# Kernel tuning notes

Measured on AMD Instinct MI355X. Metric: run time of the kernel, lower is better.

## Reference

```python
import jax, jax.numpy as jnp
import numpy as np
from jax import lax

H = 1024
W = 1024
WIN = 32
STR = 16
NH = (H - WIN) // STR + 1  # 63
N = NH * NH                # 3969 patches
DN3 = ('NCDHW', 'OIDHW', 'NCDHW')
DN2 = ('NCHW', 'OIHW', 'NCHW')


def setup_inputs() -> dict:
    key = jax.random.key(0)
    ks = jax.random.split(key, 13)
    r = lambda k, s, sc=0.05: jax.random.normal(k, s, dtype=jnp.float32) * sc
    return {
        'x1': jax.random.normal(ks[0], (1, 1, 1, H, W), jnp.float32),
        'x2': jax.random.normal(ks[1], (1, 1, 1, H, W), jnp.float32),
        'conv1_w': r(ks[2], (24, 1, 2, 8, 8)),      # Conv3d(1,24,(2,8,8)) [O,I,D,H,W]
        'conv1_b': r(ks[3], (24,)),
        'conv2_w': r(ks[4], (60, 24, 5, 5)),         # Conv2d(24,60,5)
        'conv2_b': r(ks[5], (60,)),
        'deconv2_w': r(ks[6], (60, 24, 5, 5)),       # ConvTranspose2d(60,24,5) [I,O,kH,kW]
        'deconv2_b': r(ks[7], (24,)),
        'deconv1_w': r(ks[8], (24, 1, 2, 8, 8)),     # ConvTranspose3d(24,1,(2,8,8)) [I,O,D,H,W]
        'deconv1_b': r(ks[9], (1,)),
        'lin_w': r(ks[10], (N, 2), 0.5),             # per-patch Linear(2,1) weights
        'lin_b': r(ks[11], (N,), 0.5),               # per-patch Linear(2,1) bias
        'linear1_w': r(ks[12], (1, 1), 0.5),         # Linear(1,1,bias=False)
    }


def _conv(x, w, b, dn):
    nd = w.ndim - 2
    y = lax.conv_general_dilated(x, w, (1,) * nd, 'VALID', dimension_numbers=dn)
    return y + b.reshape((1, -1) + (1,) * nd)


def _convT(x, w, b, dn):
    # stride-1, pad-0 transposed conv == full-pad conv with flipped, IO-swapped kernel
    nd = w.ndim - 2
    wf = jnp.flip(w, axis=tuple(range(2, w.ndim))).swapaxes(0, 1)  # [O,I,*k]
    pad = [(k - 1, k - 1) for k in w.shape[2:]]
    y = lax.conv_general_dilated(x, wf, (1,) * nd, pad, dimension_numbers=dn)
    return y + b.reshape((1, -1) + (1,) * nd)


def reference(x1, x2, conv1_w, conv1_b, conv2_w, conv2_b, deconv2_w, deconv2_b,
              deconv1_w, deconv1_b, lin_w, lin_b, linear1_w):
    x = jnp.concatenate([x1, x2], axis=2)[0, 0]  # [2,H,W]
    idx = (jnp.arange(NH) * STR)[:, None] + jnp.arange(WIN)[None, :]  # [NH,32]
    # unfold dims 3,4 with window 32 / stride 16 -> [2,NH,NW,32,32]
    patches = x[:, idx[:, None, :, None], idx[None, :, None, :]]
    outX = patches.reshape(2, N, WIN, WIN).transpose(1, 0, 2, 3)[:, None]  # [N,1,2,32,32]
    h = jax.nn.elu(_conv(outX, conv1_w, conv1_b, DN3))        # [N,24,1,25,25]
    h = jax.nn.relu(_conv(h[:, :, 0], conv2_w, conv2_b, DN2))  # [N,60,21,21]
    h = jax.nn.elu(_convT(h, deconv2_w, deconv2_b, DN2))       # [N,24,25,25]
    h = _convT(h[:, :, None], deconv1_w, deconv1_b, DN3)       # [N,1,2,32,32]
    # per-patch Linear(2,1) over depth channels, batched over all patches
    p = jnp.einsum('nchw,nc->nhw', h[:, 0], lin_w) + lin_b[:, None, None]  # [N,32,32]
    p = p.reshape(NH, NH, WIN, WIN)
    # col2im: overlap-add fold, block 32, stride 16 -> [H,W]
    recon = jnp.zeros((H, W), jnp.float32).at[idx[:, None, :, None], idx[None, :, None, :]].add(p)
    outX2 = recon * linear1_w[0, 0]  # Linear(1,1,bias=False) per pixel
    return x2 - outX2.reshape(x2.shape)
```

## Files before the change

### kernel.cpp

```cpp
#include <hip/hip_runtime.h>
#include <hip/hip_bf16.h>

static constexpr int H_ = 1024;
static constexpr int W_ = 1024;
static constexpr int STR_ = 16;
static constexpr int NH_ = 63;
static constexpr int NPATCH_ = NH_ * NH_;

typedef short bf16x8 __attribute__((ext_vector_type(8)));
typedef short short4v __attribute__((ext_vector_type(4)));
typedef float f32x4 __attribute__((ext_vector_type(4)));

static constexpr int SH1_STRIDE = 48;
static constexpr int SH2_BASE   = 30016;
static constexpr int SH2_STRIDE = 120;
static constexpr int ZROW_REL   = 441 * SH2_STRIDE;
static constexpr int SPB0       = 30016;
static constexpr int SPB1       = 35136;
static constexpr int SWC_BASE   = 30016;
static constexpr int SP_ACC     = 34112;
static constexpr int LDS_BYTES  = 83072;

__device__ __forceinline__ unsigned short f2bf(float x) {
    __hip_bfloat16 b = __float2bfloat16(x);
    return __builtin_bit_cast(unsigned short, b);
}

__device__ __forceinline__ f32x4 mfma_bf16(bf16x8 a, bf16x8 b, f32x4 c) {
    return __builtin_amdgcn_mfma_f32_16x16x32_bf16(a, b, c, 0, 0, 0);
}

__global__ __launch_bounds__(1024, 4) void fused_patch_kernel(
    const float* __restrict__ x1, const float* __restrict__ x2,
    const float* __restrict__ c1b, const float* __restrict__ c2b,
    const float* __restrict__ d2b, const float* __restrict__ d1b,
    const float* __restrict__ lin_w, const float* __restrict__ lin_b,
    const unsigned short* __restrict__ w1frag,
    const unsigned short* __restrict__ w2frag,
    const unsigned short* __restrict__ dw2frag,
    const float* __restrict__ dw1,
    float* __restrict__ recon)
{
    __shared__ alignas(16) char sbuf[LDS_BYTES];
    const int n  = blockIdx.x;
    const int t  = (int)threadIdx.x;
    const int pi = n / NH_, pj = n % NH_;
    const int Y0 = pi * STR_, X0 = pj * STR_;
    const int wv = t >> 6, lane = t & 63;
    const int ln15 = lane & 15, quad = lane >> 4;

    if (t < 30) ((float*)(sbuf + SH2_BASE + ZROW_REL))[t] = 0.f;
    for (int k = t; k < 2048; k += 1024) {
        int d = k >> 10, r = k & 1023, y = r >> 5, x = r & 31;
        unsigned short b = f2bf((d ? x2 : x1)[(Y0 + y) * W_ + (X0 + x)]);
        int row = (d * 32 + y) * 40;
        ((unsigned short*)(sbuf + SPB0))[row + x] = b;
        if (x > 0) ((unsigned short*)(sbuf + SPB1))[row + x - 1] = b;
    }
    __syncthreads();

    for (int tl = wv; tl < 50; tl += 16) {
        const int vcol = tl >> 1, ubase = (tl & 1) * 16;
        const int u = ubase + ln15;
        const char* abase = sbuf + ((vcol & 1) ? SPB1 : SPB0) + (vcol & ~1) * 2;
        f32x4 acc[2];
        acc[0] = (f32x4){0.f, 0.f, 0.f, 0.f};
        acc[1] = (f32x4){0.f, 0.f, 0.f, 0.f};
        #pragma unroll
        for (int kc = 0; kc < 4; ++kc) {
            const int idx8 = kc * 4 + quad;
            const int dd = idx8 >> 3, pp = idx8 & 7;
            const unsigned int* ap = (const unsigned int*)(abase + (dd * 32 + u + pp) * 80);
            union { unsigned int u4[4]; bf16x8 v; } af;
            af.u4[0] = ap[0]; af.u4[1] = ap[1]; af.u4[2] = ap[2]; af.u4[3] = ap[3];
            bf16x8 b0 = *(const bf16x8*)(w1frag + (((kc * 2 + 0) * 64) + lane) * 8);
            bf16x8 b1 = *(const bf16x8*)(w1frag + (((kc * 2 + 1) * 64) + lane) * 8);
            acc[0] = mfma_bf16(af.v, b0, acc[0]);
            acc[1] = mfma_bf16(af.v, b1, acc[1]);
        }
        #pragma unroll
        for (int ntp = 0; ntp < 2; ++ntp) {
            const int c = ntp * 16 + ln15;
            if (c < 24) {
                const float bias = c1b[c];
                #pragma unroll
                for (int r = 0; r < 4; ++r) {
                    int uu = ubase + quad * 4 + r;
                    if (uu < 25) {
                        float hv = acc[ntp][r] + bias;
                        hv = hv > 0.f ? hv : expm1f(hv);
                        *(unsigned short*)(sbuf + (uu * 25 + vcol) * SH1_STRIDE + c * 2) = f2bf(hv);
                    }
                }
            }
        }
    }
    __syncthreads();

    if (wv < 14) {
        int abase2[2];
        #pragma unroll
        for (int i = 0; i < 2; ++i) {
            int m = (wv + i * 14) * 16 + ln15;
            if (m > 440) m = 440;
            abase2[i] = ((m / 21) * 25 + (m % 21)) * SH1_STRIDE;
        }
        float bias[4];
        #pragma unroll
        for (int nt = 0; nt < 4; ++nt) {
            int o = nt * 16 + ln15;
            bias[nt] = (o < 60) ? c2b[o] : 0.f;
        }
        f32x4 acc2[2][4];
        #pragma unroll
        for (int i = 0; i < 2; ++i)
            #pragma unroll
            for (int nt = 0; nt < 4; ++nt)
                acc2[i][nt] = (f32x4){0.f, 0.f, 0.f, 0.f};

        const unsigned short* wb = w2frag + lane * 8;
        #pragma unroll
        for (int p = 0; p < 5; ++p) {
            #pragma unroll
            for (int q = 0; q < 5; ++q) {
                const int tap  = p * 5 + q;
                const int toff = (p * 25 + q) * SH1_STRIDE;
                bf16x8 b[4];
                #pragma unroll
                for (int nt = 0; nt < 4; ++nt)
                    b[nt] = *(const bf16x8*)(wb + (tap * 4 + nt) * 512);
                #pragma unroll
                for (int i = 0; i < 2; ++i) {
                    bf16x8 a = *(const bf16x8*)(sbuf + abase2[i] + toff + quad * 16);
                    #pragma unroll
                    for (int nt = 0; nt < 4; ++nt)
                        acc2[i][nt] = mfma_bf16(a, b[nt], acc2[i][nt]);
                }
            }
        }
        #pragma unroll
        for (int i = 0; i < 2; ++i) {
            #pragma unroll
            for (int r = 0; r < 4; ++r) {
                int pix = (wv + i * 14) * 16 + quad * 4 + r;
                if (pix < 441) {
                    unsigned short* rowp = (unsigned short*)(sbuf + SH2_BASE + pix * SH2_STRIDE);
                    #pragma unroll
                    for (int nt = 0; nt < 4; ++nt) {
                        int o = nt * 16 + ln15;
                        if (o < 60)
                            rowp[o] = f2bf(fmaxf(acc2[i][nt][r] + bias[nt], 0.f));
                    }
                }
            }
        }
    }
    __syncthreads();

    f32x4 acc3[3][2];
    {
        #pragma unroll
        for (int i = 0; i < 3; ++i) {
            acc3[i][0] = (f32x4){0.f, 0.f, 0.f, 0.f};
            acc3[i][1] = (f32x4){0.f, 0.f, 0.f, 0.f};
        }
        int uarr[3], varr[3], a120[3];
        bool mval[3];
        #pragma unroll
        for (int i = 0; i < 3; ++i) {
            int m = (wv + i * 16) * 16 + ln15;
            mval[i] = (m < 625);
            int mc = mval[i] ? m : 0;
            uarr[i] = mc / 25; varr[i] = mc % 25;
            a120[i] = (uarr[i] * 21 + varr[i]) * SH2_STRIDE;
        }
        const unsigned short* db = dw2frag + lane * 8;
        #pragma unroll
        for (int dy = 0; dy < 5; ++dy) {
            #pragma unroll
            for (int dx = 0; dx < 5; ++dx) {
                const int tap   = dy * 5 + dx;
                const int t2off = (dy * 21 + dx) * SH2_STRIDE;
                bf16x8 b00 = *(const bf16x8*)(db + tap * 2048);
                bf16x8 b01 = *(const bf16x8*)(db + tap * 2048 + 512);
                bf16x8 b10 = *(const bf16x8*)(db + tap * 2048 + 1024);
                bf16x8 b11 = *(const bf16x8*)(db + tap * 2048 + 1536);
                #pragma unroll
                for (int i = 0; i < 3; ++i) {
                    if (i == 2 && wv >= 8) continue;
                    int yv = uarr[i] - dy, xv = varr[i] - dx;
                    bool ok = mval[i] && ((unsigned)yv < 21u) && ((unsigned)xv < 21u);
                    int ra = ok ? (a120[i] - t2off) : ZROW_REL;
                    const char* ap = sbuf + SH2_BASE + ra + quad * 16;
                    short4v lo0 = *(const short4v*)(ap);
                    short4v hi0 = *(const short4v*)(ap + 8);
                    bf16x8 a0 = __builtin_shufflevector(lo0, hi0, 0, 1, 2, 3, 4, 5, 6, 7);
                    acc3[i][0] = mfma_bf16(a0, b00, acc3[i][0]);
                    acc3[i][1] = mfma_bf16(a0, b01, acc3[i][1]);
                    short4v lo1 = *(const short4v*)(ap + 64);
                    short4v hi1 = *(const short4v*)(ap + 72);
                    bf16x8 a1 = __builtin_shufflevector(lo1, hi1, 0, 1, 2, 3, 4, 5, 6, 7);
                    acc3[i][0] = mfma_bf16(a1, b10, acc3[i][0]);
                    acc3[i][1] = mfma_bf16(a1, b11, acc3[i][1]);
                }
            }
        }
    }
    __syncthreads();

    const float lw0 = lin_w[2 * n], lw1 = lin_w[2 * n + 1];
    float* sp = (float*)(sbuf + SP_ACC);
    {
        const int c0 = ln15, c1 = 16 + ln15;
        const float db0 = d2b[c0];
        const float db1 = (c1 < 24) ? d2b[c1] : 0.f;
        #pragma unroll
        for (int i = 0; i < 3; ++i) {
            if (i == 2 && wv >= 8) continue;
            #pragma unroll
            for (int r = 0; r < 4; ++r) {
                int pix = (wv + i * 16) * 16 + quad * 4 + r;
                if (pix < 625) {
                    unsigned short* rowp = (unsigned short*)(sbuf + pix * SH1_STRIDE);
                    float hv = acc3[i][0][r] + db0;
                    rowp[c0] = f2bf(hv > 0.f ? hv : expm1f(hv));
                    if (c1 < 24) {
                        float hw = acc3[i][1][r] + db1;
                        rowp[c1] = f2bf(hw > 0.f ? hw : expm1f(hw));
                    }
                }
            }
        }
    }
    for (int k = t; k < 2048; k += 1024) {
        int r = k >> 5, c = k & 31;
        float v = 0.f;
        if (c < 24)
            v = lw0 * dw1[(c * 2 + 0) * 64 + r] + lw1 * dw1[(c * 2 + 1) * 64 + r];
        ((unsigned short*)(sbuf + SWC_BASE))[r * 32 + c] = f2bf(v);
    }
    sp[t] = 0.f;
    __syncthreads();

    {
        bf16x8 wbv[4];
        #pragma unroll
        for (int nt = 0; nt < 4; ++nt)
            wbv[nt] = *(const bf16x8*)(sbuf + SWC_BASE + (nt * 16 + ln15) * 64 + quad * 16);
        #pragma unroll
        for (int i = 0; i < 3; ++i) {
            int mt = wv + i * 16;
            if (mt >= 40) continue;
            int m = mt * 16 + ln15;
            if (m > 624) m = 624;
            bf16x8 a = *(const bf16x8*)(sbuf + m * SH1_STRIDE + quad * 16);
            #pragma unroll
            for (int nt = 0; nt < 4; ++nt) {
                f32x4 acc4 = (f32x4){0.f, 0.f, 0.f, 0.f};
                acc4 = mfma_bf16(a, wbv[nt], acc4);
                #pragma unroll
                for (int r = 0; r < 4; ++r) {
                    int pix = mt * 16 + quad * 4 + r;
                    if (pix < 625) {
                        int u = pix / 25, v = pix % 25;
                        int rv = nt * 16 + ln15;
                        atomicAdd(&sp[(u + (rv >> 3)) * 32 + v + (rv & 7)], acc4[r]);
                    }
                }
            }
        }
    }
    __syncthreads();

    const float obias = d1b[0] * (lw0 + lw1) + lin_b[n];
    {
        int yy = t >> 5, xx = t & 31;
        atomicAdd(&recon[(Y0 + yy) * W_ + (X0 + xx)], sp[t] + obias);
    }
}

__global__ void prep_kernel(const float* __restrict__ c1w,
                            const float* __restrict__ c2w,
                            const float* __restrict__ d2w,
                            unsigned short* __restrict__ w1frag,
                            unsigned short* __restrict__ w2frag,
                            unsigned short* __restrict__ dw2frag)
{
    int i = blockIdx.x * blockDim.x + threadIdx.x;
    if (i < 51200) {
        int j = i & 7, lane = (i >> 3) & 63;
        int ln15 = lane & 15, quad = lane >> 4;
        if (i < 4096) {
            int g = i >> 9;
            int kc = g >> 1, nt = g & 1;
            int nn = nt * 16 + ln15, k = kc * 32 + quad * 8 + j;
            w1frag[i] = f2bf((nn < 24) ? c1w[nn * 128 + k] : 0.f);
        }
        {
            int nt = (i >> 9) & 3, tap = i >> 11;
            int o = nt * 16 + ln15, c = quad * 8 + j;
            float v = (o < 60 && c < 24) ? c2w[(o * 24 + c) * 25 + tap] : 0.f;
            w2frag[i] = f2bf(v);
        }
        {
            int nt = (i >> 9) & 1, kc = (i >> 10) & 1, tap = i >> 11;
            int k = kc * 32 + quad * 8 + j, c = nt * 16 + ln15;
            float v = (k < 60 && c < 24) ? d2w[(k * 24 + c) * 25 + tap] : 0.f;
            dw2frag[i] = f2bf(v);
        }
    }
}

__global__ void finalize_kernel(const float* __restrict__ x2,
                                const float* __restrict__ l1w,
                                float* __restrict__ out)
{
    int i = blockIdx.x * blockDim.x + threadIdx.x;
    if (i < H_ * W_) {
        float r = out[i];
        out[i] = x2[i] - r * l1w[0];
    }
}

extern "C" void kernel_launch(void* const* d_in, const int* in_sizes, int n_in,
                              void* d_out, int out_size, void* d_ws, size_t ws_size,
                              hipStream_t stream)
{
    const float* x1  = (const float*)d_in[0];
    const float* x2  = (const float*)d_in[1];
    const float* c1w = (const float*)d_in[2];
    const float* c1b = (const float*)d_in[3];
    const float* c2w = (const float*)d_in[4];
    const float* c2b = (const float*)d_in[5];
    const float* d2w = (const float*)d_in[6];
    const float* d2b = (const float*)d_in[7];
    const float* d1w = (const float*)d_in[8];
    const float* d1b = (const float*)d_in[9];
    const float* lw  = (const float*)d_in[10];
    const float* lb  = (const float*)d_in[11];
    const float* l1w = (const float*)d_in[12];

    float*          out     = (float*)d_out;
    unsigned short* w1frag  = (unsigned short*)d_ws;
    unsigned short* w2frag  = (unsigned short*)((char*)d_ws + 8192);
    unsigned short* dw2frag = (unsigned short*)((char*)d_ws + 110592);

    hipMemsetAsync(d_out, 0, (size_t)H_ * W_ * sizeof(float), stream);
    prep_kernel<<<100, 512, 0, stream>>>(c1w, c2w, d2w, w1frag, w2frag, dw2frag);
    fused_patch_kernel<<<NPATCH_, 1024, 0, stream>>>(x1, x2, c1b, c2b, d2b, d1b,
                                                     lw, lb, w1frag, w2frag, dw2frag,
                                                     d1w, out);
    finalize_kernel<<<(H_ * W_ + 255) / 256, 256, 0, stream>>>(x2, l1w, out);
}
```

Baseline: 1.435 ms.

## Compute conv1 once over full image and stream it to per-patch kernel

Adds a kernel that computes the first conv+ELU over the whole image into a global bf16 workspace, removing the fourfold redundant conv1 work across overlapping patches. The per-patch kernel then reads conv2 inputs directly from global memory, uses 512 threads and a smaller LDS footprint. The new path runs only when the workspace is large enough; otherwise the old fused kernel is used. It trades recomputation for about 50MB of extra global traffic and uncached-LDS reads in conv2.

New measurement: 3.090 ms. 2.15x slower.

```diff
diff --git a/kernel.cpp b/kernel.cpp
--- a/kernel.cpp
+++ b/kernel.cpp
@@ -6,31 +6,298 @@
 static constexpr int STR_ = 16;
 static constexpr int NH_ = 63;
 static constexpr int NPATCH_ = NH_ * NH_;
+static constexpr int HO_ = 1017;
 
 typedef short bf16x8 __attribute__((ext_vector_type(8)));
 typedef short short4v __attribute__((ext_vector_type(4)));
 typedef float f32x4 __attribute__((ext_vector_type(4)));
 
-static constexpr int SH1_STRIDE = 48;
-static constexpr int SH2_BASE   = 30016;
-static constexpr int SH2_STRIDE = 120;
-static constexpr int ZROW_REL   = 441 * SH2_STRIDE;
-static constexpr int SPB0       = 30016;
-static constexpr int SPB1       = 35136;
-static constexpr int SWC_BASE   = 30016;
-static constexpr int SP_ACC     = 34112;
-static constexpr int LDS_BYTES  = 83072;
+static constexpr size_t WS_FRAGS   = 212992;
+static constexpr int    H1_XSTRIDE = 48;
+static constexpr int    H1_YSTRIDE = 1024 * 48;
+static constexpr size_t H1_BYTES   = (size_t)HO_ * H1_YSTRIDE;
+static constexpr size_t WS_NEED_A  = WS_FRAGS + H1_BYTES;
 
 __device__ __forceinline__ unsigned short f2bf(float x) {
     __hip_bfloat16 b = __float2bfloat16(x);
     return __builtin_bit_cast(unsigned short, b);
 }
-
 __device__ __forceinline__ f32x4 mfma_bf16(bf16x8 a, bf16x8 b, f32x4 c) {
     return __builtin_amdgcn_mfma_f32_16x16x32_bf16(a, b, c, 0, 0, 0);
 }
 
-__global__ __launch_bounds__(1024, 4) void fused_patch_kernel(
+
+__global__ __launch_bounds__(512, 4) void conv1_full_kernel(
+    const float* __restrict__ x1, const float* __restrict__ x2,
+    const float* __restrict__ c1b,
+    const unsigned short* __restrict__ w1frag,
+    unsigned short* __restrict__ h1full)
+{
+    __shared__ alignas(16) unsigned short spb[2 * 2 * 39 * 40];
+    unsigned short* copy0 = spb;
+    unsigned short* copy1 = spb + 2 * 39 * 40;
+
+    const int b  = blockIdx.x;
+    const int by = b >> 5, bx = b & 31;
+    const int y0 = by * 32, x0 = bx * 32;
+    const int t  = (int)threadIdx.x;
+    const int wv = t >> 6, lane = t & 63;
+    const int ln15 = lane & 15, quad = lane >> 4;
+
+    for (int k = t; k < 2 * 39 * 39; k += 512) {
+        int d = k / 1521, r = k % 1521, yy = r / 39, xx = r % 39;
+        int gy = y0 + yy; if (gy > 1023) gy = 1023;
+        int gx = x0 + xx; if (gx > 1023) gx = 1023;
+        unsigned short v = f2bf((d ? x2 : x1)[gy * W_ + gx]);
+        int row = (d * 39 + yy) * 40;
+        copy0[row + xx] = v;
+        if (xx > 0) copy1[row + xx - 1] = v;
+    }
+    __syncthreads();
+
+    bf16x8 bw[4][2];
+    #pragma unroll
+    for (int kc = 0; kc < 4; ++kc)
+        #pragma unroll
+        for (int nt = 0; nt < 2; ++nt)
+            bw[kc][nt] = *(const bf16x8*)(w1frag + (((kc * 2 + nt) * 64) + lane) * 8);
+
+    for (int tl = wv; tl < 64; tl += 8) {
+        const int vcol = tl >> 1, ubase = (tl & 1) * 16;
+        const int u = ubase + ln15;
+        const char* abase = (const char*)((vcol & 1) ? copy1 : copy0) + (vcol & ~1) * 2;
+        f32x4 acc[2];
+        acc[0] = (f32x4){0.f, 0.f, 0.f, 0.f};
+        acc[1] = (f32x4){0.f, 0.f, 0.f, 0.f};
+        #pragma unroll
+        for (int kc = 0; kc < 4; ++kc) {
+            const int idx8 = kc * 4 + quad;
+            const int dd = idx8 >> 3, pp = idx8 & 7;
+            const unsigned int* ap = (const unsigned int*)(abase + (dd * 39 + u + pp) * 80);
+            union { unsigned int u4[4]; bf16x8 v; } af;
+            af.u4[0] = ap[0]; af.u4[1] = ap[1]; af.u4[2] = ap[2]; af.u4[3] = ap[3];
+            acc[0] = mfma_bf16(af.v, bw[kc][0], acc[0]);
+            acc[1] = mfma_bf16(af.v, bw[kc][1], acc[1]);
+        }
+        const int xg = x0 + vcol;
+        #pragma unroll
+        for (int ntp = 0; ntp < 2; ++ntp) {
+            const int c = ntp * 16 + ln15;
+            if (c < 24) {
+                const float bias = c1b[c];
+                #pragma unroll
+                for (int r = 0; r < 4; ++r) {
+                    int yg = y0 + ubase + quad * 4 + r;
+                    if (yg < HO_ && xg < HO_) {
+                        float hv = acc[ntp][r] + bias;
+                        hv = hv > 0.f ? hv : expm1f(hv);
+                        h1full[(yg * 1024 + xg) * 24 + c] = f2bf(hv);
+                    }
+                }
+            }
+        }
+    }
+}
+
+static constexpr int A_SH2_STRIDE = 120;
+static constexpr int A_ZROW  = 52920;
+static constexpr int A_SWC   = 53056;
+static constexpr int A_SP    = 57152;
+static constexpr int A_LDS   = 61248;
+static constexpr int A_H3STR = 48;
+
+__global__ __launch_bounds__(512, 4) void fused_patch_global(
+    const float* __restrict__ c2b, const float* __restrict__ d2b,
+    const float* __restrict__ d1b,
+    const float* __restrict__ lin_w, const float* __restrict__ lin_b,
+    const unsigned short* __restrict__ h1full,
+    const unsigned short* __restrict__ w2frag,
+    const unsigned short* __restrict__ dw2frag,
+    const float* __restrict__ dw1,
+    float* __restrict__ recon)
+{
+    __shared__ alignas(16) char sbuf[A_LDS];
+    const int n  = blockIdx.x;
+    const int t  = (int)threadIdx.x;
+    const int pi = n / NH_, pj = n % NH_;
+    const int Y0 = pi * STR_, X0 = pj * STR_;
+    const int wv = t >> 6, lane = t & 63;
+    const int ln15 = lane & 15, quad = lane >> 4;
+
+    if (t < 34) ((float*)(sbuf + A_ZROW))[t] = 0.f;
+
+    float bias2[4];
+    #pragma unroll
+    for (int nt = 0; nt < 4; ++nt) {
+        int o = nt * 16 + ln15;
+        bias2[nt] = (o < 60) ? c2b[o] : 0.f;
+    }
+    for (int mt = wv; mt < 28; mt += 8) {
+        int m = mt * 16 + ln15;
+        if (m > 440) m = 440;
+        int hy = m / 21, hx = m % 21;
+        const char* abase = (const char*)h1full
+                          + ((Y0 + hy) * 1024 + (X0 + hx)) * H1_XSTRIDE + quad * 16;
+        f32x4 acc[4];
+        #pragma unroll
+        for (int nt = 0; nt < 4; ++nt) acc[nt] = (f32x4){0.f, 0.f, 0.f, 0.f};
+        const unsigned short* wb = w2frag + lane * 8;
+        #pragma unroll
+        for (int p = 0; p < 5; ++p) {
+            #pragma unroll
+            for (int q = 0; q < 5; ++q) {
+                const int tap = p * 5 + q;
+                bf16x8 a = *(const bf16x8*)(abase + p * H1_YSTRIDE + q * H1_XSTRIDE);
+                #pragma unroll
+                for (int nt = 0; nt < 4; ++nt) {
+                    bf16x8 bb = *(const bf16x8*)(wb + (tap * 4 + nt) * 512);
+                    acc[nt] = mfma_bf16(a, bb, acc[nt]);
+                }
+            }
+        }
+        #pragma unroll
+        for (int r = 0; r < 4; ++r) {
+            int pix = mt * 16 + quad * 4 + r;
+            if (pix < 441) {
+                unsigned short* rowp = (unsigned short*)(sbuf + pix * A_SH2_STRIDE);
+                #pragma unroll
+                for (int nt = 0; nt < 4; ++nt) {
+                    int o = nt * 16 + ln15;
+                    if (o < 60)
+                        rowp[o] = f2bf(fmaxf(acc[nt][r] + bias2[nt], 0.f));
+                }
+            }
+        }
+    }
+    __syncthreads();
+
+    f32x4 acc3[5][2];
+    {
+        int uarr[5], varr[5], a120[5];
+        bool mval[5];
+        #pragma unroll
+        for (int i = 0; i < 5; ++i) {
+            acc3[i][0] = (f32x4){0.f, 0.f, 0.f, 0.f};
+            acc3[i][1] = (f32x4){0.f, 0.f, 0.f, 0.f};
+            int m = (wv + i * 8) * 16 + ln15;
+            mval[i] = (m < 625);
+            int mc = mval[i] ? m : 0;
+            uarr[i] = mc / 25; varr[i] = mc % 25;
+            a120[i] = (uarr[i] * 21 + varr[i]) * A_SH2_STRIDE;
+        }
+        const unsigned short* db = dw2frag + lane * 8;
+        #pragma unroll
+        for (int dy = 0; dy < 5; ++dy) {
+            #pragma unroll
+            for (int dx = 0; dx < 5; ++dx) {
+                const int tap   = dy * 5 + dx;
+                const int t2off = (dy * 21 + dx) * A_SH2_STRIDE;
+                bf16x8 b00 = *(const bf16x8*)(db + tap * 2048);
+                bf16x8 b01 = *(const bf16x8*)(db + tap * 2048 + 512);
+                bf16x8 b10 = *(const bf16x8*)(db + tap * 2048 + 1024);
+                bf16x8 b11 = *(const bf16x8*)(db + tap * 2048 + 1536);
+                #pragma unroll
+                for (int i = 0; i < 5; ++i) {
+                    int yv = uarr[i] - dy, xv = varr[i] - dx;
+                    bool ok = mval[i] && ((unsigned)yv < 21u) && ((unsigned)xv < 21u);
+                    int ra = ok ? (a120[i] - t2off) : A_ZROW;
+                    const char* ap = sbuf + ra + quad * 16;
+                    short4v lo0 = *(const short4v*)(ap);
+                    short4v hi0 = *(const short4v*)(ap + 8);
+                    bf16x8 a0 = __builtin_shufflevector(lo0, hi0, 0, 1, 2, 3, 4, 5, 6, 7);
+                    acc3[i][0] = mfma_bf16(a0, b00, acc3[i][0]);
+                    acc3[i][1] = mfma_bf16(a0, b01, acc3[i][1]);
+                    short4v lo1 = *(const short4v*)(ap + 64);
+                    short4v hi1 = *(const short4v*)(ap + 72);
+                    bf16x8 a1 = __builtin_shufflevector(lo1, hi1, 0, 1, 2, 3, 4, 5, 6, 7);
+                    acc3[i][0] = mfma_bf16(a1, b10, acc3[i][0]);
+                    acc3[i][1] = mfma_bf16(a1, b11, acc3[i][1]);
+                }
+            }
+        }
+    }
+    __syncthreads();
+
+    const float lw0 = lin_w[2 * n], lw1 = lin_w[2 * n + 1];
+    float* sp = (float*)(sbuf + A_SP);
+    {
+        const int c0 = ln15, c1 = 16 + ln15;
+        const float db0 = d2b[c0];
+        const float db1 = (c1 < 24) ? d2b[c1] : 0.f;
+        #pragma unroll
+        for (int i = 0; i < 5; ++i) {
+            #pragma unroll
+            for (int r = 0; r < 4; ++r) {
+                int pix = (wv + i * 8) * 16 + quad * 4 + r;
+                if (pix < 625) {
+                    unsigned short* rowp = (unsigned short*)(sbuf + pix * A_H3STR);
+                    float hv = acc3[i][0][r] + db0;
+                    rowp[c0] = f2bf(hv > 0.f ? hv : expm1f(hv));
+                    if (c1 < 24) {
+                        float hw = acc3[i][1][r] + db1;
+                        rowp[c1] = f2bf(hw > 0.f ? hw : expm1f(hw));
+                    }
+                }
+            }
+        }
+    }
+    for (int k = t; k < 2048; k += 512) {
+        int r = k >> 5, c = k & 31;
+        float v = 0.f;
+        if (c < 24)
+            v = lw0 * dw1[(c * 2 + 0) * 64 + r] + lw1 * dw1[(c * 2 + 1) * 64 + r];
+        ((unsigned short*)(sbuf + A_SWC))[r * 32 + c] = f2bf(v);
+    }
+    for (int k = t; k < 1024; k += 512) sp[k] = 0.f;
+    __syncthreads();
+
+    {
+        bf16x8 wbv[4];
+        #pragma unroll
+        for (int nt = 0; nt < 4; ++nt)
+            wbv[nt] = *(const bf16x8*)(sbuf + A_SWC + (nt * 16 + ln15) * 64 + quad * 16);
+        #pragma unroll
+        for (int i = 0; i < 5; ++i) {
+            int mt = wv + i * 8;
+            int m = mt * 16 + ln15;
+            if (m > 624) m = 624;
+            bf16x8 a = *(const bf16x8*)(sbuf + m * A_H3STR + quad * 16);
+            #pragma unroll
+            for (int nt = 0; nt < 4; ++nt) {
+                f32x4 acc4 = (f32x4){0.f, 0.f, 0.f, 0.f};
+                acc4 = mfma_bf16(a, wbv[nt], acc4);
+                #pragma unroll
+                for (int r = 0; r < 4; ++r) {
+                    int pix = mt * 16 + quad * 4 + r;
+                    if (pix < 625) {
+                        int u = pix / 25, v = pix % 25;
+                        int rv = nt * 16 + ln15;
+                        atomicAdd(&sp[(u + (rv >> 3)) * 32 + v + (rv & 7)], acc4[r]);
+                    }
+                }
+            }
+        }
+    }
+    __syncthreads();
+
+    const float obias = d1b[0] * (lw0 + lw1) + lin_b[n];
+    for (int k = t; k < 1024; k += 512) {
+        int yy = k >> 5, xx = k & 31;
+        atomicAdd(&recon[(Y0 + yy) * W_ + (X0 + xx)], sp[k] + obias);
+    }
+}
+
+static constexpr int B_SH1_STRIDE = 48;
+static constexpr int B_SH2_BASE   = 30016;
+static constexpr int B_SH2_STRIDE = 120;
+static constexpr int B_ZROW_REL   = 441 * B_SH2_STRIDE;
+static constexpr int B_SPB0       = 30016;
+static constexpr int B_SPB1       = 35136;
+static constexpr int B_SWC_BASE   = 30016;
+static constexpr int B_SP_ACC     = 34112;
+static constexpr int B_LDS_BYTES  = 83072;
+
+__global__ __launch_bounds__(1024, 4) void fused_patch_local(
     const float* __restrict__ x1, const float* __restrict__ x2,
     const float* __restrict__ c1b, const float* __restrict__ c2b,
     const float* __restrict__ d2b, const float* __restrict__ d1b,
@@ -41,7 +308,7 @@
     const float* __restrict__ dw1,
     float* __restrict__ recon)
 {
-    __shared__ alignas(16) char sbuf[LDS_BYTES];
+    __shared__ alignas(16) char sbuf[B_LDS_BYTES];
     const int n  = blockIdx.x;
     const int t  = (int)threadIdx.x;
     const int pi = n / NH_, pj = n % NH_;
@@ -49,20 +316,20 @@
     const int wv = t >> 6, lane = t & 63;
     const int ln15 = lane & 15, quad = lane >> 4;
 
-    if (t < 30) ((float*)(sbuf + SH2_BASE + ZROW_REL))[t] = 0.f;
+    if (t < 30) ((float*)(sbuf + B_SH2_BASE + B_ZROW_REL))[t] = 0.f;
     for (int k = t; k < 2048; k += 1024) {
         int d = k >> 10, r = k & 1023, y = r >> 5, x = r & 31;
         unsigned short b = f2bf((d ? x2 : x1)[(Y0 + y) * W_ + (X0 + x)]);
         int row = (d * 32 + y) * 40;
-        ((unsigned short*)(sbuf + SPB0))[row + x] = b;
-        if (x > 0) ((unsigned short*)(sbuf + SPB1))[row + x - 1] = b;
+        ((unsigned short*)(sbuf + B_SPB0))[row + x] = b;
+        if (x > 0) ((unsigned short*)(sbuf + B_SPB1))[row + x - 1] = b;
     }
     __syncthreads();
 
     for (int tl = wv; tl < 50; tl += 16) {
         const int vcol = tl >> 1, ubase = (tl & 1) * 16;
         const int u = ubase + ln15;
-        const char* abase = sbuf + ((vcol & 1) ? SPB1 : SPB0) + (vcol & ~1) * 2;
+        const char* abase = sbuf + ((vcol & 1) ? B_SPB1 : B_SPB0) + (vcol & ~1) * 2;
         f32x4 acc[2];
         acc[0] = (f32x4){0.f, 0.f, 0.f, 0.f};
         acc[1] = (f32x4){0.f, 0.f, 0.f, 0.f};
@@ -89,7 +356,7 @@
                     if (uu < 25) {
                         float hv = acc[ntp][r] + bias;
                         hv = hv > 0.f ? hv : expm1f(hv);
-                        *(unsigned short*)(sbuf + (uu * 25 + vcol) * SH1_STRIDE + c * 2) = f2bf(hv);
+                        *(unsigned short*)(sbuf + (uu * 25 + vcol) * B_SH1_STRIDE + c * 2) = f2bf(hv);
                     }
                 }
             }
@@ -103,7 +370,7 @@
         for (int i = 0; i < 2; ++i) {
             int m = (wv + i * 14) * 16 + ln15;
             if (m > 440) m = 440;
-            abase2[i] = ((m / 21) * 25 + (m % 21)) * SH1_STRIDE;
+            abase2[i] = ((m / 21) * 25 + (m % 21)) * B_SH1_STRIDE;
         }
         float bias[4];
         #pragma unroll
@@ -124,7 +391,7 @@
             #pragma unroll
             for (int q = 0; q < 5; ++q) {
                 const int tap  = p * 5 + q;
-                const int toff = (p * 25 + q) * SH1_STRIDE;
+                const int toff = (p * 25 + q) * B_SH1_STRIDE;
                 bf16x8 b[4];
                 #pragma unroll
                 for (int nt = 0; nt < 4; ++nt)
@@ -144,7 +411,7 @@
             for (int r = 0; r < 4; ++r) {
                 int pix = (wv + i * 14) * 16 + quad * 4 + r;
                 if (pix < 441) {
-                    unsigned short* rowp = (unsigned short*)(sbuf + SH2_BASE + pix * SH2_STRIDE);
+                    unsigned short* rowp = (unsigned short*)(sbuf + B_SH2_BASE + pix * B_SH2_STRIDE);
                     #pragma unroll
                     for (int nt = 0; nt < 4; ++nt) {
                         int o = nt * 16 + ln15;
@@ -172,7 +439,7 @@
             mval[i] = (m < 625);
             int mc = mval[i] ? m : 0;
             uarr[i] = mc / 25; varr[i] = mc % 25;
-            a120[i] = (uarr[i] * 21 + varr[i]) * SH2_STRIDE;
+            a120[i] = (uarr[i] * 21 + varr[i]) * B_SH2_STRIDE;
         }
         const unsigned short* db = dw2frag + lane * 8;
         #pragma unroll
@@ -180,7 +447,7 @@
             #pragma unroll
             for (int dx = 0; dx < 5; ++dx) {
                 const int tap   = dy * 5 + dx;
-                const int t2off = (dy * 21 + dx) * SH2_STRIDE;
+                const int t2off = (dy * 21 + dx) * B_SH2_STRIDE;
                 bf16x8 b00 = *(const bf16x8*)(db + tap * 2048);
                 bf16x8 b01 = *(const bf16x8*)(db + tap * 2048 + 512);
                 bf16x8 b10 = *(const bf16x8*)(db + tap * 2048 + 1024);
@@ -190,8 +457,8 @@
                     if (i == 2 && wv >= 8) continue;
                     int yv = uarr[i] - dy, xv = varr[i] - dx;
                     bool ok = mval[i] && ((unsigned)yv < 21u) && ((unsigned)xv < 21u);
-                    int ra = ok ? (a120[i] - t2off) : ZROW_REL;
-                    const char* ap = sbuf + SH2_BASE + ra + quad * 16;
+                    int ra = ok ? (a120[i] - t2off) : B_ZROW_REL;
+                    const char* ap = sbuf + B_SH2_BASE + ra + quad * 16;
                     short4v lo0 = *(const short4v*)(ap);
                     short4v hi0 = *(const short4v*)(ap + 8);
                     bf16x8 a0 = __builtin_shufflevector(lo0, hi0, 0, 1, 2, 3, 4, 5, 6, 7);
@@ -209,7 +476,7 @@
     __syncthreads();
 
     const float lw0 = lin_w[2 * n], lw1 = lin_w[2 * n + 1];
-    float* sp = (float*)(sbuf + SP_ACC);
+    float* sp = (float*)(sbuf + B_SP_ACC);
     {
         const int c0 = ln15, c1 = 16 + ln15;
         const float db0 = d2b[c0];
@@ -221,7 +488,7 @@
             for (int r = 0; r < 4; ++r) {
                 int pix = (wv + i * 16) * 16 + quad * 4 + r;
                 if (pix < 625) {
-                    unsigned short* rowp = (unsigned short*)(sbuf + pix * SH1_STRIDE);
+                    unsigned short* rowp = (unsigned short*)(sbuf + pix * B_SH1_STRIDE);
                     float hv = acc3[i][0][r] + db0;
                     rowp[c0] = f2bf(hv > 0.f ? hv : expm1f(hv));
                     if (c1 < 24) {
@@ -237,7 +504,7 @@
         float v = 0.f;
         if (c < 24)
             v = lw0 * dw1[(c * 2 + 0) * 64 + r] + lw1 * dw1[(c * 2 + 1) * 64 + r];
-        ((unsigned short*)(sbuf + SWC_BASE))[r * 32 + c] = f2bf(v);
+        ((unsigned short*)(sbuf + B_SWC_BASE))[r * 32 + c] = f2bf(v);
     }
     sp[t] = 0.f;
     __syncthreads();
@@ -246,14 +513,14 @@
         bf16x8 wbv[4];
         #pragma unroll
         for (int nt = 0; nt < 4; ++nt)
-            wbv[nt] = *(const bf16x8*)(sbuf + SWC_BASE + (nt * 16 + ln15) * 64 + quad * 16);
+            wbv[nt] = *(const bf16x8*)(sbuf + B_SWC_BASE + (nt * 16 + ln15) * 64 + quad * 16);
         #pragma unroll
         for (int i = 0; i < 3; ++i) {
             int mt = wv + i * 16;
             if (mt >= 40) continue;
             int m = mt * 16 + ln15;
             if (m > 624) m = 624;
-            bf16x8 a = *(const bf16x8*)(sbuf + m * SH1_STRIDE + quad * 16);
+            bf16x8 a = *(const bf16x8*)(sbuf + m * B_SH1_STRIDE + quad * 16);
             #pragma unroll
             for (int nt = 0; nt < 4; ++nt) {
                 f32x4 acc4 = (f32x4){0.f, 0.f, 0.f, 0.f};
@@ -340,15 +607,24 @@
     const float* lb  = (const float*)d_in[11];
     const float* l1w = (const float*)d_in[12];
 
-    float*          out     = (float*)d_out;
+    float* out = (float*)d_out;
     unsigned short* w1frag  = (unsigned short*)d_ws;
     unsigned short* w2frag  = (unsigned short*)((char*)d_ws + 8192);
     unsigned short* dw2frag = (unsigned short*)((char*)d_ws + 110592);
+    unsigned short* h1full  = (unsigned short*)((char*)d_ws + WS_FRAGS);
 
     hipMemsetAsync(d_out, 0, (size_t)H_ * W_ * sizeof(float), stream);
     prep_kernel<<<100, 512, 0, stream>>>(c1w, c2w, d2w, w1frag, w2frag, dw2frag);
-    fused_patch_kernel<<<NPATCH_, 1024, 0, stream>>>(x1, x2, c1b, c2b, d2b, d1b,
-                                                     lw, lb, w1frag, w2frag, dw2frag,
-                                                     d1w, out);
+
+    if (ws_size >= WS_NEED_A) {
+        conv1_full_kernel<<<1024, 512, 0, stream>>>(x1, x2, c1b, w1frag, h1full);
+        fused_patch_global<<<NPATCH_, 512, 0, stream>>>(c2b, d2b, d1b, lw, lb,
+                                                        h1full, w2frag, dw2frag,
+                                                        d1w, out);
+    } else {
+        fused_patch_local<<<NPATCH_, 1024, 0, stream>>>(x1, x2, c1b, c2b, d2b, d1b,
+                                                        lw, lb, w1frag, w2frag, dw2frag,
+                                                        d1w, out);
+    }
     finalize_kernel<<<(H_ * W_ + 255) / 256, 256, 0, stream>>>(x2, l1w, out);
 }
```
